# Kernel tuning notes

Hardware: AMD Instinct MI355X
Metric: run time of the kernel (lower is better)

## Reference

```python
import jax, jax.numpy as jnp
import numpy as np

T = 0.4       # gumbel temperature (self.T)
BASE = 3.0    # sigmoid offset (self.base)
LN_EPS = 1e-5


def setup_inputs() -> dict:
    key = jax.random.key(0)
    ks = jax.random.split(key, 4)
    B, S, D = 2, 2048, 4096
    E, EMB, M = 64, 128, 11008
    return {
        "x": jax.random.normal(ks[0], (B, S, D), dtype=jnp.float32),
        "rnn_state": jax.random.normal(ks[1], (E, EMB), dtype=jnp.float32),
        "Wr": jax.random.normal(ks[2], (E, D), dtype=jnp.float32) * 0.02,
        "Wd": jax.random.normal(ks[3], (M, EMB), dtype=jnp.float32) * 0.02,
        "ln_w": jnp.ones((EMB,), dtype=jnp.float32),
        "ln_b": jnp.zeros((EMB,), dtype=jnp.float32),
    }


def _layernorm(h, w, b):
    mu = jnp.mean(h, axis=-1, keepdims=True)
    var = jnp.var(h, axis=-1, keepdims=True)
    return (h - mu) * jax.lax.rsqrt(var + LN_EPS) * w + b


def reference(x, rnn_state, Wr, Wd, ln_w, ln_b):
    key = jax.random.key(42)
    k1, k2 = jax.random.split(key)
    # router logits: [B, S, E]
    logits = jnp.einsum("bsd,ed->bse", x, Wr)
    # ST gumbel-softmax (hard one-hot routing)
    eps = 1e-20
    u = jax.random.uniform(k1, logits.shape, dtype=logits.dtype)
    g = -jnp.log(-jnp.log(u + eps) + eps)
    y_soft = jax.nn.softmax((logits + g) / T, axis=-1)
    y_hard = jax.nn.one_hot(jnp.argmax(y_soft, axis=-1), logits.shape[-1], dtype=y_soft.dtype)
    router = jax.lax.stop_gradient(y_hard - y_soft) + y_soft
    # gather routed embedding: [B, S, EMB]
    routed = jnp.einsum("bse,ec->bsc", router, rnn_state)
    # LN + GELU (exact erf) + decode: [B, S, M]
    h = jax.nn.gelu(_layernorm(routed, ln_w, ln_b), approximate=False)
    pre = jnp.einsum("bsc,mc->bsm", h, Wd)
    # ST gumbel-sigmoid with offset, hard round
    e = jax.random.exponential(k2, pre.shape, dtype=pre.dtype)
    gum = -jnp.log(e)
    b_soft = jax.nn.sigmoid((pre + gum + BASE) / T)
    b_hard = jnp.round(b_soft)
    binary = jax.lax.stop_gradient(b_hard - b_soft) + b_soft
    return (binary, router)
```

## Files before the change

kernel.cpp:

```cpp
#include <hip/hip_runtime.h>
#include <hip/hip_bf16.h>
#include <stdint.h>

typedef float floatx4 __attribute__((ext_vector_type(4)));

__host__ __device__ inline uint32_t rotl32(uint32_t x, int r) {
#ifdef __HIP_DEVICE_COMPILE__
  return __builtin_amdgcn_alignbit(x, x, 32 - r);
#else
  return (x << r) | (x >> (32 - r));
#endif
}

__host__ __device__ inline void tf2x32(uint32_t k0, uint32_t k1,
                                       uint32_t x0, uint32_t x1,
                                       uint32_t& o0, uint32_t& o1) {
  const uint32_t k2 = k0 ^ k1 ^ 0x1BD11BDAu;
  x0 += k0; x1 += k1;
#define TFR(r) { x0 += x1; x1 = rotl32(x1, r); x1 ^= x0; }
  TFR(13) TFR(15) TFR(26) TFR(6)
  x0 += k1; x1 += k2 + 1u;
  TFR(17) TFR(29) TFR(16) TFR(24)
  x0 += k2; x1 += k0 + 2u;
  TFR(13) TFR(15) TFR(26) TFR(6)
  x0 += k0; x1 += k1 + 3u;
  TFR(17) TFR(29) TFR(16) TFR(24)
  x0 += k1; x1 += k2 + 4u;
  TFR(13) TFR(15) TFR(26) TFR(6)
  x0 += k2; x1 += k0 + 5u;
#undef TFR
  o0 = x0; o1 = x1;
}

__device__ inline uint32_t jax_bits32(uint32_t kA, uint32_t kB, uint32_t i) {
  uint32_t o0, o1;
  tf2x32(kA, kB, 0u, i, o0, o1);
  return o0 ^ o1;
}

__device__ inline float jax_uniform(uint32_t bits) {
  return __uint_as_float((bits >> 9) | 0x3f800000u) - 1.0f;
}

#define D_DIM   4096
#define E_DIM   64
#define EMB     128
#define M_DIM   11008
#define NROWS   4096
#define BIN_N   45088768
#define KSPLIT  32
#define CK      32
#define XSTR    284
#define WSTR    68

__device__ inline int qspread(int v) { return v + ((v >> 5) << 2); }

__global__ __launch_bounds__(256) void krnA(const float* __restrict__ x,
                                            const float* __restrict__ Wr,
                                            float* __restrict__ part) {
  __shared__ __align__(16) float xsT[CK * XSTR];
  __shared__ __align__(16) float wsT[CK * WSTR];
  const int rb = blockIdx.x, ks = blockIdx.y, t = threadIdx.x;
  const int rbase = rb * 256, kbase0 = ks * 128;
  const int jc = t & 7, rg = t >> 3;
  const int xoff = (rg * 8) + ((rg >> 2) << 2);
  const int woff = (jc * 8) + ((jc >> 2) << 2);
  float acc[8][8] = {};

  for (int c = 0; c < 4; ++c) {
    const int kbase = kbase0 + c * CK;
#pragma unroll
    for (int it = 0; it < 8; ++it) {
      int idx = t + it * 256;
      int row = idx >> 3, kq = idx & 7;
      float4 v = *(const float4*)&x[(size_t)(rbase + row) * D_DIM + kbase + kq * 4];
      int adr = qspread(row);
      xsT[(kq * 4 + 0) * XSTR + adr] = v.x;
      xsT[(kq * 4 + 1) * XSTR + adr] = v.y;
      xsT[(kq * 4 + 2) * XSTR + adr] = v.z;
      xsT[(kq * 4 + 3) * XSTR + adr] = v.w;
    }
#pragma unroll
    for (int it = 0; it < 2; ++it) {
      int idx = t + it * 256;
      int e = idx >> 3, kq = idx & 7;
      float4 v = *(const float4*)&Wr[(size_t)e * D_DIM + kbase + kq * 4];
      int adr = qspread(e);
      wsT[(kq * 4 + 0) * WSTR + adr] = v.x;
      wsT[(kq * 4 + 1) * WSTR + adr] = v.y;
      wsT[(kq * 4 + 2) * WSTR + adr] = v.z;
      wsT[(kq * 4 + 3) * WSTR + adr] = v.w;
    }
    __syncthreads();
#pragma unroll
    for (int k = 0; k < CK; ++k) {
      const float* xp = &xsT[k * XSTR + xoff];
      const float* wp = &wsT[k * WSTR + woff];
      floatx4 xa = *(const floatx4*)xp;
      floatx4 xb = *(const floatx4*)(xp + 4);
      floatx4 wa = *(const floatx4*)wp;
      floatx4 wb = *(const floatx4*)(wp + 4);
#pragma unroll
      for (int r = 0; r < 4; ++r)
#pragma unroll
        for (int e = 0; e < 4; ++e) {
          acc[r][e]         += xa[r] * wa[e];
          acc[r][e + 4]     += xa[r] * wb[e];
          acc[r + 4][e]     += xb[r] * wa[e];
          acc[r + 4][e + 4] += xb[r] * wb[e];
        }
    }
    __syncthreads();
  }
#pragma unroll
  for (int r = 0; r < 8; ++r) {
    float* pp = part + ((size_t)ks * NROWS + rbase + rg * 8 + r) * E_DIM + jc * 8;
    *(float4*)pp = make_float4(acc[r][0], acc[r][1], acc[r][2], acc[r][3]);
    *(float4*)(pp + 4) = make_float4(acc[r][4], acc[r][5], acc[r][6], acc[r][7]);
  }
}

__global__ __launch_bounds__(256) void krnB(const float* __restrict__ part,
                                            float* __restrict__ router_out,
                                            int* __restrict__ eidx,
                                            uint32_t K1A, uint32_t K1B) {
  const int t = threadIdx.x;
  const int wv = t >> 6, lane = t & 63;
  const int row = blockIdx.x * 4 + wv;
  float lg = 0.0f;
#pragma unroll
  for (int s = 0; s < KSPLIT; ++s)
    lg += part[((size_t)s * NROWS + row) * E_DIM + lane];

  uint32_t jf = (uint32_t)row * 64u + (uint32_t)lane;
  uint32_t bits = jax_bits32(K1A, K1B, jf);
  float u = jax_uniform(bits);
  float inner = -logf(u + 1e-20f);
  float g = -logf(inner + 1e-20f);
  float w = (lg + g) * 2.5f;

  float m = w;
#pragma unroll
  for (int off = 32; off >= 1; off >>= 1) m = fmaxf(m, __shfl_xor(m, off));
  unsigned long long msk = __ballot(w == m);
  int arg = __ffsll(msk) - 1;
  router_out[(size_t)row * E_DIM + lane] = (lane == arg) ? 1.0f : 0.0f;
  if (lane == 0) eidx[row] = arg;
}

__global__ __launch_bounds__(64) void krnC1(const float* __restrict__ rnn,
                                            const float* __restrict__ lnw,
                                            const float* __restrict__ lnb,
                                            float* __restrict__ H,
                                            uint32_t* __restrict__ pminKey) {
  const int r = blockIdx.x, lane = threadIdx.x;
  if (r == 0 && lane == 0) *pminKey = 0xFFFFFFFFu;
  float v0 = rnn[r * EMB + lane], v1 = rnn[r * EMB + 64 + lane];
  float s = v0 + v1;
#pragma unroll
  for (int off = 32; off >= 1; off >>= 1) s += __shfl_xor(s, off);
  float mu = s * (1.0f / 128.0f);
  float d0 = v0 - mu, d1 = v1 - mu;
  float q = d0 * d0 + d1 * d1;
#pragma unroll
  for (int off = 32; off >= 1; off >>= 1) q += __shfl_xor(q, off);
  float var = q * (1.0f / 128.0f);
  float rs = rsqrtf(var + 1e-5f);
  float h0 = d0 * rs * lnw[lane] + lnb[lane];
  float h1 = d1 * rs * lnw[lane + 64] + lnb[lane + 64];
  float g0 = 0.5f * h0 * (1.0f + erff(h0 * 0.70710678118654752f));
  float g1 = 0.5f * h1 * (1.0f + erff(h1 * 0.70710678118654752f));
  H[r * EMB + lane] = g0;
  H[r * EMB + 64 + lane] = g1;
}

__device__ inline uint32_t fkey(float f) {
  uint32_t b = __float_as_uint(f);
  return (b & 0x80000000u) ? ~b : (b | 0x80000000u);
}

__global__ __launch_bounds__(256) void krnC2(const float* __restrict__ H,
                                             const float* __restrict__ Wd,
                                             float* __restrict__ P,
                                             uint32_t* __restrict__ pminKey) {
  __shared__ float4 hs[64][32];
  const int t = threadIdx.x;
#pragma unroll
  for (int it = 0; it < 8; ++it) {
    int idx = t + it * 256;
    hs[idx >> 5][idx & 31] = ((const float4*)H)[idx];
  }
  __syncthreads();
  const int wv = t >> 6, lane = t & 63;
  const int m = blockIdx.x * 64 + lane;
  const float4* wd4 = (const float4*)(Wd + (size_t)m * EMB);
  float acc[16] = {};
  for (int c4 = 0; c4 < 32; ++c4) {
    float4 w = wd4[c4];
#pragma unroll
    for (int e = 0; e < 16; ++e) {
      float4 h = hs[wv * 16 + e][c4];
      acc[e] += w.x * h.x + w.y * h.y + w.z * h.z + w.w * h.w;
    }
  }
  float mn = acc[0];
#pragma unroll
  for (int e = 0; e < 16; ++e) {
    P[(size_t)(wv * 16 + e) * M_DIM + m] = acc[e];
    mn = fminf(mn, acc[e]);
  }
#pragma unroll
  for (int off = 32; off >= 1; off >>= 1)
    mn = fminf(mn, __shfl_xor(mn, off));
  if (lane == 0) atomicMin(pminKey, fkey(mn));
}

__device__ inline float decide(float pre, uint32_t bits) {
  float u = jax_uniform(bits);
  float om = 1.0f - u;
  float e = -__logf(om);
  float gum = -__logf(e);
  float z = pre + gum + 3.0f;
  return (z > 0.0f) ? 1.0f : 0.0f;
}

__global__ __launch_bounds__(256) void krnD(const float* __restrict__ P,
                                            const int* __restrict__ eidx,
                                            const uint32_t* __restrict__ pminKey,
                                            float* __restrict__ out,
                                            uint32_t K2A, uint32_t K2B) {
  uint32_t kk = *pminKey;
  uint32_t pb = (kk & 0x80000000u) ? (kk ^ 0x80000000u) : ~kk;
  float pmin = __uint_as_float(pb);
  float tt = pmin + 2.95f;
  float delta = __expf(-__expf(tt));
  delta = fminf(fmaxf(delta, 1.2e-7f), 0.5f);
  uint32_t Ku = (uint32_t)((1.0f - delta) * 8388608.0f);
  uint32_t K9 = Ku << 9;

  uint32_t g = (blockIdx.x * 256u + threadIdx.x) * 4u;
  uint32_t b0 = jax_bits32(K2A, K2B, g + 0u);
  uint32_t b1 = jax_bits32(K2A, K2B, g + 1u);
  uint32_t b2 = jax_bits32(K2A, K2B, g + 2u);
  uint32_t b3 = jax_bits32(K2A, K2B, g + 3u);
  floatx4 r = {1.0f, 1.0f, 1.0f, 1.0f};
  uint32_t mx = max(max(b0, b1), max(b2, b3));
  if (mx >= K9) {
    uint32_t row = g / (uint32_t)M_DIM;
    uint32_t m = g - row * (uint32_t)M_DIM;
    const float* pp = &P[(size_t)eidx[row] * M_DIM + m];
    if (b0 >= K9) r.x = decide(pp[0], b0);
    if (b1 >= K9) r.y = decide(pp[1], b1);
    if (b2 >= K9) r.z = decide(pp[2], b2);
    if (b3 >= K9) r.w = decide(pp[3], b3);
  }
  __builtin_nontemporal_store(r, (floatx4*)&out[g]);
}

extern "C" void kernel_launch(void* const* d_in, const int* in_sizes, int n_in,
                              void* d_out, int out_size, void* d_ws, size_t ws_size,
                              hipStream_t stream) {
  const float* x    = (const float*)d_in[0];
  const float* rnn  = (const float*)d_in[1];
  const float* Wr   = (const float*)d_in[2];
  const float* Wd   = (const float*)d_in[3];
  const float* lnw  = (const float*)d_in[4];
  const float* lnb  = (const float*)d_in[5];
  float* out = (float*)d_out;

  uint32_t K1A, K1B, K2A, K2B;
  tf2x32(0u, 42u, 0u, 0u, K1A, K1B);
  tf2x32(0u, 42u, 0u, 1u, K2A, K2B);

  char* ws = (char*)d_ws;
  int*      eidx    = (int*)ws;
  float*    H       = (float*)(ws + 16384);
  float*    P       = (float*)(ws + 65536);
  uint32_t* pminKey = (uint32_t*)(ws + 3276800);

  float* part = out;
  float* router_out = out + (size_t)BIN_N;

  krnA<<<dim3(16, KSPLIT), 256, 0, stream>>>(x, Wr, part);
  krnB<<<1024, 256, 0, stream>>>(part, router_out, eidx, K1A, K1B);
  krnC1<<<64, 64, 0, stream>>>(rnn, lnw, lnb, H, pminKey);
  krnC2<<<172, 256, 0, stream>>>(H, Wd, P, pminKey);
  krnD<<<44032, 256, 0, stream>>>(P, eidx, pminKey, out, K2A, K2B);
}
```

Baseline: 334.5 us.

## Fuse LN+GELU into decode GEMM, drop atomics, reorder partial-sum layout

Computes the LayerNorm and GELU of rnn_state inside each krnC2 block, which removes the separate krnC1 launch and the H buffer. The atomicMin is replaced by per-block minima that krnB's first block reduces; that block also computes the K9 threshold once instead of every krnD thread recomputing it. The split-K partial logits are now stored row-major per row, so krnB's 32-way reduction reads contiguous memory. The cost is redundant LN+GELU work in every krnC2 block and an extra serial tail in krnB block 0.

Result: no change. 328.5 us (-1.8%).

```diff
diff --git a/kernel.cpp b/kernel.cpp
--- a/kernel.cpp
+++ b/kernel.cpp
@@ -52,6 +52,7 @@
 #define CK      32
 #define XSTR    284
 #define WSTR    68
+#define C2BLKS  172
 
 __device__ inline int qspread(int v) { return v + ((v >> 5) << 2); }
 
@@ -114,81 +115,57 @@
   }
 #pragma unroll
   for (int r = 0; r < 8; ++r) {
-    float* pp = part + ((size_t)ks * NROWS + rbase + rg * 8 + r) * E_DIM + jc * 8;
+    float* pp = part + ((size_t)(rbase + rg * 8 + r) * KSPLIT + ks) * E_DIM + jc * 8;
     *(float4*)pp = make_float4(acc[r][0], acc[r][1], acc[r][2], acc[r][3]);
     *(float4*)(pp + 4) = make_float4(acc[r][4], acc[r][5], acc[r][6], acc[r][7]);
   }
 }
 
-__global__ __launch_bounds__(256) void krnB(const float* __restrict__ part,
-                                            float* __restrict__ router_out,
-                                            int* __restrict__ eidx,
-                                            uint32_t K1A, uint32_t K1B) {
-  const int t = threadIdx.x;
-  const int wv = t >> 6, lane = t & 63;
-  const int row = blockIdx.x * 4 + wv;
-  float lg = 0.0f;
-#pragma unroll
-  for (int s = 0; s < KSPLIT; ++s)
-    lg += part[((size_t)s * NROWS + row) * E_DIM + lane];
-
-  uint32_t jf = (uint32_t)row * 64u + (uint32_t)lane;
-  uint32_t bits = jax_bits32(K1A, K1B, jf);
-  float u = jax_uniform(bits);
-  float inner = -logf(u + 1e-20f);
-  float g = -logf(inner + 1e-20f);
-  float w = (lg + g) * 2.5f;
-
-  float m = w;
-#pragma unroll
-  for (int off = 32; off >= 1; off >>= 1) m = fmaxf(m, __shfl_xor(m, off));
-  unsigned long long msk = __ballot(w == m);
-  int arg = __ffsll(msk) - 1;
-  router_out[(size_t)row * E_DIM + lane] = (lane == arg) ? 1.0f : 0.0f;
-  if (lane == 0) eidx[row] = arg;
-}
-
-__global__ __launch_bounds__(64) void krnC1(const float* __restrict__ rnn,
-                                            const float* __restrict__ lnw,
-                                            const float* __restrict__ lnb,
-                                            float* __restrict__ H,
-                                            uint32_t* __restrict__ pminKey) {
-  const int r = blockIdx.x, lane = threadIdx.x;
-  if (r == 0 && lane == 0) *pminKey = 0xFFFFFFFFu;
-  float v0 = rnn[r * EMB + lane], v1 = rnn[r * EMB + 64 + lane];
-  float s = v0 + v1;
-#pragma unroll
-  for (int off = 32; off >= 1; off >>= 1) s += __shfl_xor(s, off);
-  float mu = s * (1.0f / 128.0f);
-  float d0 = v0 - mu, d1 = v1 - mu;
-  float q = d0 * d0 + d1 * d1;
-#pragma unroll
-  for (int off = 32; off >= 1; off >>= 1) q += __shfl_xor(q, off);
-  float var = q * (1.0f / 128.0f);
-  float rs = rsqrtf(var + 1e-5f);
-  float h0 = d0 * rs * lnw[lane] + lnb[lane];
-  float h1 = d1 * rs * lnw[lane + 64] + lnb[lane + 64];
-  float g0 = 0.5f * h0 * (1.0f + erff(h0 * 0.70710678118654752f));
-  float g1 = 0.5f * h1 * (1.0f + erff(h1 * 0.70710678118654752f));
-  H[r * EMB + lane] = g0;
-  H[r * EMB + 64 + lane] = g1;
-}
-
-__device__ inline uint32_t fkey(float f) {
-  uint32_t b = __float_as_uint(f);
-  return (b & 0x80000000u) ? ~b : (b | 0x80000000u);
-}
-
-__global__ __launch_bounds__(256) void krnC2(const float* __restrict__ H,
+__global__ __launch_bounds__(256) void krnC2(const float* __restrict__ rnn,
+                                             const float* __restrict__ lnw,
+                                             const float* __restrict__ lnb,
                                              const float* __restrict__ Wd,
                                              float* __restrict__ P,
-                                             uint32_t* __restrict__ pminKey) {
-  __shared__ float4 hs[64][32];
+                                             float* __restrict__ pminLoc) {
+  __shared__ float4 hs[64][33];
+  __shared__ float rmin[4];
   const int t = threadIdx.x;
-#pragma unroll
-  for (int it = 0; it < 8; ++it) {
-    int idx = t + it * 256;
-    hs[idx >> 5][idx & 31] = ((const float4*)H)[idx];
+  {
+    const int r = t >> 2, q = t & 3;
+    const float4* rp = (const float4*)(rnn + r * EMB) + q * 8;
+    float4 v[8];
+    float s = 0.0f;
+#pragma unroll
+    for (int j = 0; j < 8; ++j) {
+      v[j] = rp[j];
+      s += v[j].x + v[j].y + v[j].z + v[j].w;
+    }
+    s += __shfl_xor(s, 1); s += __shfl_xor(s, 2);
+    const float mu = s * (1.0f / 128.0f);
+    float qs = 0.0f;
+#pragma unroll
+    for (int j = 0; j < 8; ++j) {
+      float dx = v[j].x - mu, dy = v[j].y - mu, dz = v[j].z - mu, dw = v[j].w - mu;
+      qs += dx * dx + dy * dy + dz * dz + dw * dw;
+    }
+    qs += __shfl_xor(qs, 1); qs += __shfl_xor(qs, 2);
+    const float rs = rsqrtf(qs * (1.0f / 128.0f) + 1e-5f);
+    const float4* wp = (const float4*)lnw + q * 8;
+    const float4* bp = (const float4*)lnb + q * 8;
+#pragma unroll
+    for (int j = 0; j < 8; ++j) {
+      float4 w = wp[j], b = bp[j], g;
+      float h;
+      h = (v[j].x - mu) * rs * w.x + b.x;
+      g.x = 0.5f * h * (1.0f + erff(h * 0.70710678118654752f));
+      h = (v[j].y - mu) * rs * w.y + b.y;
+      g.y = 0.5f * h * (1.0f + erff(h * 0.70710678118654752f));
+      h = (v[j].z - mu) * rs * w.z + b.z;
+      g.z = 0.5f * h * (1.0f + erff(h * 0.70710678118654752f));
+      h = (v[j].w - mu) * rs * w.w + b.w;
+      g.w = 0.5f * h * (1.0f + erff(h * 0.70710678118654752f));
+      hs[r][q * 8 + j] = g;
+    }
   }
   __syncthreads();
   const int wv = t >> 6, lane = t & 63;
@@ -212,7 +189,57 @@
 #pragma unroll
   for (int off = 32; off >= 1; off >>= 1)
     mn = fminf(mn, __shfl_xor(mn, off));
-  if (lane == 0) atomicMin(pminKey, fkey(mn));
+  if (lane == 0) rmin[wv] = mn;
+  __syncthreads();
+  if (t == 0)
+    pminLoc[blockIdx.x] = fminf(fminf(rmin[0], rmin[1]), fminf(rmin[2], rmin[3]));
+}
+
+__global__ __launch_bounds__(256) void krnB(const float* __restrict__ part,
+                                            float* __restrict__ router_out,
+                                            int* __restrict__ eidx,
+                                            const float* __restrict__ pminLoc,
+                                            uint32_t* __restrict__ K9out,
+                                            uint32_t K1A, uint32_t K1B) {
+  __shared__ float red[4];
+  const int t = threadIdx.x;
+  const int wv = t >> 6, lane = t & 63;
+  const int row = blockIdx.x * 4 + wv;
+  float lg = 0.0f;
+#pragma unroll
+  for (int s = 0; s < KSPLIT; ++s)
+    lg += part[((size_t)row * KSPLIT + s) * E_DIM + lane];
+
+  uint32_t jf = (uint32_t)row * 64u + (uint32_t)lane;
+  uint32_t bits = jax_bits32(K1A, K1B, jf);
+  float u = jax_uniform(bits);
+  float inner = -logf(u + 1e-20f);
+  float g = -logf(inner + 1e-20f);
+  float w = (lg + g) * 2.5f;
+
+  float m = w;
+#pragma unroll
+  for (int off = 32; off >= 1; off >>= 1) m = fmaxf(m, __shfl_xor(m, off));
+  unsigned long long msk = __ballot(w == m);
+  int arg = __ffsll(msk) - 1;
+  router_out[(size_t)row * E_DIM + lane] = (lane == arg) ? 1.0f : 0.0f;
+  if (lane == 0) eidx[row] = arg;
+
+  if (blockIdx.x == 0) {
+    float v = (t < C2BLKS) ? pminLoc[t] : 3.0e38f;
+#pragma unroll
+    for (int off = 32; off >= 1; off >>= 1) v = fminf(v, __shfl_xor(v, off));
+    if (lane == 0) red[wv] = v;
+    __syncthreads();
+    if (t == 0) {
+      float pmin = fminf(fminf(red[0], red[1]), fminf(red[2], red[3]));
+      float tt = pmin + 2.95f;
+      float delta = __expf(-__expf(tt));
+      delta = fminf(fmaxf(delta, 1.2e-7f), 0.5f);
+      uint32_t Ku = (uint32_t)((1.0f - delta) * 8388608.0f);
+      *K9out = Ku << 9;
+    }
+  }
 }
 
 __device__ inline float decide(float pre, uint32_t bits) {
@@ -226,17 +253,10 @@
 
 __global__ __launch_bounds__(256) void krnD(const float* __restrict__ P,
                                             const int* __restrict__ eidx,
-                                            const uint32_t* __restrict__ pminKey,
+                                            const uint32_t* __restrict__ K9p,
                                             float* __restrict__ out,
                                             uint32_t K2A, uint32_t K2B) {
-  uint32_t kk = *pminKey;
-  uint32_t pb = (kk & 0x80000000u) ? (kk ^ 0x80000000u) : ~kk;
-  float pmin = __uint_as_float(pb);
-  float tt = pmin + 2.95f;
-  float delta = __expf(-__expf(tt));
-  delta = fminf(fmaxf(delta, 1.2e-7f), 0.5f);
-  uint32_t Ku = (uint32_t)((1.0f - delta) * 8388608.0f);
-  uint32_t K9 = Ku << 9;
+  const uint32_t K9 = *K9p;
 
   uint32_t g = (blockIdx.x * 256u + threadIdx.x) * 4u;
   uint32_t b0 = jax_bits32(K2A, K2B, g + 0u);
@@ -274,16 +294,15 @@
 
   char* ws = (char*)d_ws;
   int*      eidx    = (int*)ws;
-  float*    H       = (float*)(ws + 16384);
   float*    P       = (float*)(ws + 65536);
-  uint32_t* pminKey = (uint32_t*)(ws + 3276800);
+  float*    pminLoc = (float*)(ws + 2990080);
+  uint32_t* K9u     = (uint32_t*)(ws + 2991104);
 
   float* part = out;
   float* router_out = out + (size_t)BIN_N;
 
   krnA<<<dim3(16, KSPLIT), 256, 0, stream>>>(x, Wr, part);
-  krnB<<<1024, 256, 0, stream>>>(part, router_out, eidx, K1A, K1B);
-  krnC1<<<64, 64, 0, stream>>>(rnn, lnw, lnb, H, pminKey);
-  krnC2<<<172, 256, 0, stream>>>(H, Wd, P, pminKey);
-  krnD<<<44032, 256, 0, stream>>>(P, eidx, pminKey, out, K2A, K2B);
-}
+  krnC2<<<C2BLKS, 256, 0, stream>>>(rnn, lnw, lnb, Wd, P, pminLoc);
+  krnB<<<1024, 256, 0, stream>>>(part, router_out, eidx, pminLoc, K9u, K1A, K1B);
+  krnD<<<44032, 256, 0, stream>>>(P, eidx, K9u, out, K2A, K2B);
+}
```
